# Performance work log

Measured on AMD Instinct MI355X. Metric: run time of the kernel, lower is better.

## Reference

```python
import jax, jax.numpy as jnp
import numpy as np

N = 100000      # n_heads + n_tails (graph nodes)
E = 1600000     # nnz of sparse adjacency A_in
D = 128         # in_dim == out_dim == embed_dim
LAMDA = 0.5
ALPHA = 0.1
LAYER = 1
LN_EPS = 1e-5
LEAKY_SLOPE = 0.01


def setup_inputs() -> dict:
    key = jax.random.key(0)
    ks = jax.random.split(key, 12)
    glorot = lambda k, shape: jax.random.uniform(
        k, shape, jnp.float32, -1.0, 1.0) * np.sqrt(6.0 / (shape[0] + shape[1]))
    stdv = 1.0 / np.sqrt(D)
    return {
        "ego_embeddings": jax.random.normal(ks[0], (N, D), jnp.float32),
        "h0": jax.random.normal(ks[1], (N, D), jnp.float32),  # all_layers[0]
        "vals": jax.random.uniform(ks[2], (E,), jnp.float32),
        "row": jax.random.randint(ks[3], (E,), 0, N, jnp.int32),
        "col": jax.random.randint(ks[4], (E,), 0, N, jnp.int32),
        # nn.Parameter weight (in_dim, in_dim), uniform(-stdv, stdv)
        "weight": jax.random.uniform(ks[5], (D, D), jnp.float32, -stdv, stdv),
        # linear_h0: embed_dim -> in_dim
        "w_h0": glorot(ks[6], (D, D)),
        "b_h0": jnp.zeros((D,), jnp.float32),
        # linear: in_dim -> out_dim
        "w_lin": glorot(ks[7], (D, D)),
        "b_lin": jnp.zeros((D,), jnp.float32),
        # LayerNorm(out_dim)
        "gamma": jnp.ones((D,), jnp.float32),
        "beta_ln": jnp.zeros((D,), jnp.float32),
    }


def _layernorm(x, g, b):
    mu = jnp.mean(x, axis=-1, keepdims=True)
    var = jnp.mean(jnp.square(x - mu), axis=-1, keepdims=True)
    return (x - mu) * jax.lax.rsqrt(var + LN_EPS) * g + b


def reference(ego_embeddings, h0, vals, weight, w_h0, b_h0, w_lin, b_lin,
              gamma, beta_ln, row, col):
    n = ego_embeddings.shape[0]
    # side_embeddings = A_in @ ego_embeddings  (sparse COO SpMM)
    msgs = vals[:, None] * ego_embeddings[col]          # [E, D] gather
    side = jax.ops.segment_sum(msgs, row, num_segments=n)
    # gcn aggregator
    hi = ego_embeddings + side
    # residual_connection with identity mapping (GCNII-style)
    h0p = h0 @ w_h0.T + b_h0
    residual = (1.0 - ALPHA) * hi + ALPHA * h0p
    beta = float(np.log(LAMDA / LAYER + 1.0))
    identity_mapping = (1.0 - beta) + beta * weight     # [D, D]
    emb = residual @ identity_mapping
    # linear + LeakyReLU
    emb = jax.nn.leaky_relu(emb @ w_lin.T + b_lin, LEAKY_SLOPE)
    # LayerNorm; dropout p=0 -> identity
    return _layernorm(emb, gamma, beta_ln)
```

## Files before the change

### kernel.cpp

```cpp
#include <hip/hip_runtime.h>

#define DD 128
#define SLOTS 64

typedef float  nf4 __attribute__((ext_vector_type(4)));
typedef int    ni4 __attribute__((ext_vector_type(4)));

__global__ void scatter_k(const int* __restrict__ rowi, const int* __restrict__ coli,
                          const float* __restrict__ vals, int* __restrict__ cnt,
                          int2* __restrict__ edgeS, int E) {
  int e = (blockIdx.x * 256 + threadIdx.x) * 4;
  if (e + 3 < E) {
    ni4 r = __builtin_nontemporal_load((const ni4*)(rowi + e));
    ni4 c = __builtin_nontemporal_load((const ni4*)(coli + e));
    nf4 v = __builtin_nontemporal_load((const nf4*)(vals + e));
    int p0 = atomicAdd(&cnt[r.x], 1);
    int p1 = atomicAdd(&cnt[r.y], 1);
    int p2 = atomicAdd(&cnt[r.z], 1);
    int p3 = atomicAdd(&cnt[r.w], 1);
    if (p0 < SLOTS) edgeS[(size_t)r.x * SLOTS + p0] = make_int2(c.x, __float_as_int(v.x));
    if (p1 < SLOTS) edgeS[(size_t)r.y * SLOTS + p1] = make_int2(c.y, __float_as_int(v.y));
    if (p2 < SLOTS) edgeS[(size_t)r.z * SLOTS + p2] = make_int2(c.z, __float_as_int(v.z));
    if (p3 < SLOTS) edgeS[(size_t)r.w * SLOTS + p3] = make_int2(c.w, __float_as_int(v.w));
  } else {
    for (int j = 0; j < 4; ++j) {
      if (e + j < E) {
        int r = rowi[e + j];
        int p = atomicAdd(&cnt[r], 1);
        if (p < SLOTS) edgeS[(size_t)r * SLOTS + p] =
            make_int2(coli[e + j], __float_as_int(vals[e + j]));
      }
    }
  }
}

__global__ void w2_k(const float* __restrict__ weight, const float* __restrict__ w_lin,
                     float* __restrict__ W2) {
  const float BETA = 0.40546510810816438f;
  int idx = blockIdx.x * 256 + threadIdx.x;
  int i = idx >> 7, j = idx & 127;
  const float* wi = weight + i * DD;
  const float* lj = w_lin + j * DD;
  float s = 0.f;
#pragma unroll 8
  for (int k = 0; k < DD; ++k) s = fmaf(fmaf(BETA, wi[k], 1.0f - BETA), lj[k], s);
  W2[idx] = s;
}

__global__ void wt_k(const float* __restrict__ W2, const float* __restrict__ w_h0,
                     const float* __restrict__ b_h0, const float* __restrict__ b_lin,
                     float* __restrict__ Wf, float* __restrict__ cvec) {
  int idx = blockIdx.x * 256 + threadIdx.x;
  if (idx < 16384) {
    Wf[idx] = 0.9f * W2[idx];
  } else if (idx < 32768) {
    int t = idx - 16384;
    int p = t >> 7, n = t & 127;
    float s = 0.f;
#pragma unroll 8
    for (int k = 0; k < DD; ++k) s = fmaf(w_h0[k * DD + p], W2[k * DD + n], s);
    Wf[(128 + p) * DD + n] = 0.1f * s;
  } else if (idx < 32896) {
    int n = idx - 32768;
    float s = 0.f;
    for (int k = 0; k < DD; ++k) s = fmaf(b_h0[k], W2[k * DD + n], s);
    cvec[n] = fmaf(0.1f, s, b_lin[n]);
  }
}

__global__ __launch_bounds__(256) void fused_k(
    const float* __restrict__ ego, const int2* __restrict__ edgeS,
    const int* __restrict__ cntp, const float* __restrict__ h0,
    const float* __restrict__ Wf, const float* __restrict__ cvec,
    const float* __restrict__ gamma, const float* __restrict__ betaln,
    float* __restrict__ out, int n) {
  __shared__ float lds[4][1024];
  int wave = threadIdx.x >> 6;
  int lane = threadIdx.x & 63;
  int half = lane >> 5;
  int q = lane & 31;
  float* xs = &lds[wave][0];
  int row0 = blockIdx.x * 16 + wave * 4;
  const float4* eg4 = (const float4*)ego;
  const nf4* h4 = (const nf4*)h0;

#pragma unroll
  for (int t = 0; t < 4; ++t) {
    int r = row0 + t;
    if (r >= n) r = n - 1;
    float4 acc = (half == 0) ? eg4[(size_t)r * 32 + q] : (float4){0.f, 0.f, 0.f, 0.f};
    float4 acc2 = {0.f, 0.f, 0.f, 0.f};
    nf4 hrow = __builtin_nontemporal_load(h4 + (size_t)r * 32 + q);
    int cnt = cntp[r];
    if (cnt > SLOTS) cnt = SLOTS;
    const int2* row_edges = edgeS + (size_t)r * SLOTS;
    int mcol = 0;
    float mval = 0.f;
    if (lane < cnt) {
      int2 m = row_edges[lane];
      mcol = m.x;
      mval = __int_as_float(m.y);
    }
    int npair = (cnt + 1) >> 1;
    int j = 0;
    for (; j + 4 <= npair; j += 4) {
      int i0 = 2 * j + half;
      int c0 = __shfl(mcol, i0, 64);
      int c1 = __shfl(mcol, i0 + 2, 64);
      int c2 = __shfl(mcol, i0 + 4, 64);
      int c3 = __shfl(mcol, i0 + 6, 64);
      float v0 = __shfl(mval, i0, 64);
      float v1 = __shfl(mval, i0 + 2, 64);
      float v2 = __shfl(mval, i0 + 4, 64);
      float v3 = __shfl(mval, i0 + 6, 64);
      float4 g0 = eg4[(size_t)c0 * 32 + q];
      float4 g1 = eg4[(size_t)c1 * 32 + q];
      float4 g2 = eg4[(size_t)c2 * 32 + q];
      float4 g3 = eg4[(size_t)c3 * 32 + q];
      acc.x  = fmaf(v0, g0.x, acc.x);  acc.y  = fmaf(v0, g0.y, acc.y);
      acc.z  = fmaf(v0, g0.z, acc.z);  acc.w  = fmaf(v0, g0.w, acc.w);
      acc2.x = fmaf(v1, g1.x, acc2.x); acc2.y = fmaf(v1, g1.y, acc2.y);
      acc2.z = fmaf(v1, g1.z, acc2.z); acc2.w = fmaf(v1, g1.w, acc2.w);
      acc.x  = fmaf(v2, g2.x, acc.x);  acc.y  = fmaf(v2, g2.y, acc.y);
      acc.z  = fmaf(v2, g2.z, acc.z);  acc.w  = fmaf(v2, g2.w, acc.w);
      acc2.x = fmaf(v3, g3.x, acc2.x); acc2.y = fmaf(v3, g3.y, acc2.y);
      acc2.z = fmaf(v3, g3.z, acc2.z); acc2.w = fmaf(v3, g3.w, acc2.w);
    }
    if (j + 2 <= npair) {
      int i0 = 2 * j + half;
      int c0 = __shfl(mcol, i0, 64);
      int c1 = __shfl(mcol, i0 + 2, 64);
      float v0 = __shfl(mval, i0, 64);
      float v1 = __shfl(mval, i0 + 2, 64);
      float4 g0 = eg4[(size_t)c0 * 32 + q];
      float4 g1 = eg4[(size_t)c1 * 32 + q];
      acc.x  = fmaf(v0, g0.x, acc.x);  acc.y  = fmaf(v0, g0.y, acc.y);
      acc.z  = fmaf(v0, g0.z, acc.z);  acc.w  = fmaf(v0, g0.w, acc.w);
      acc2.x = fmaf(v1, g1.x, acc2.x); acc2.y = fmaf(v1, g1.y, acc2.y);
      acc2.z = fmaf(v1, g1.z, acc2.z); acc2.w = fmaf(v1, g1.w, acc2.w);
      j += 2;
    }
    if (j < npair) {
      int i0 = 2 * j + half;
      int c0 = __shfl(mcol, i0, 64);
      float v0 = __shfl(mval, i0, 64);
      float4 g0 = eg4[(size_t)c0 * 32 + q];
      acc.x = fmaf(v0, g0.x, acc.x); acc.y = fmaf(v0, g0.y, acc.y);
      acc.z = fmaf(v0, g0.z, acc.z); acc.w = fmaf(v0, g0.w, acc.w);
    }
    acc.x += acc2.x; acc.y += acc2.y; acc.z += acc2.z; acc.w += acc2.w;
    acc.x += __shfl_xor(acc.x, 32, 64);
    acc.y += __shfl_xor(acc.y, 32, 64);
    acc.z += __shfl_xor(acc.z, 32, 64);
    acc.w += __shfl_xor(acc.w, 32, 64);
    if (half == 0) {
      *(float4*)(xs + t * 256 + 4 * q) = acc;
    } else {
      *(float4*)(xs + t * 256 + 128 + 4 * q) =
          (float4){hrow.x, hrow.y, hrow.z, hrow.w};
    }
  }

  float acc0[4], acc1[4];
#pragma unroll
  for (int r = 0; r < 4; ++r) { acc0[r] = 0.f; acc1[r] = 0.f; }

  for (int kb = 0; kb < 64; ++kb) {
    int k = kb * 4;
    float wA0 = Wf[(k + 0) * DD + lane];
    float wA1 = Wf[(k + 1) * DD + lane];
    float wA2 = Wf[(k + 2) * DD + lane];
    float wA3 = Wf[(k + 3) * DD + lane];
    float wB0 = Wf[(k + 0) * DD + 64 + lane];
    float wB1 = Wf[(k + 1) * DD + 64 + lane];
    float wB2 = Wf[(k + 2) * DD + 64 + lane];
    float wB3 = Wf[(k + 3) * DD + 64 + lane];
#pragma unroll
    for (int r = 0; r < 4; ++r) {
      float4 xv = *(const float4*)(xs + r * 256 + k);
      acc0[r] = fmaf(xv.x, wA0, acc0[r]);
      acc0[r] = fmaf(xv.y, wA1, acc0[r]);
      acc0[r] = fmaf(xv.z, wA2, acc0[r]);
      acc0[r] = fmaf(xv.w, wA3, acc0[r]);
      acc1[r] = fmaf(xv.x, wB0, acc1[r]);
      acc1[r] = fmaf(xv.y, wB1, acc1[r]);
      acc1[r] = fmaf(xv.z, wB2, acc1[r]);
      acc1[r] = fmaf(xv.w, wB3, acc1[r]);
    }
  }

  float cb0 = cvec[lane], cb1 = cvec[64 + lane];
#pragma unroll
  for (int r = 0; r < 4; ++r) {
    float t0 = acc0[r] + cb0;
    t0 = (t0 > 0.f) ? t0 : 0.01f * t0;
    float t1 = acc1[r] + cb1;
    t1 = (t1 > 0.f) ? t1 : 0.01f * t1;
    xs[r * 132 + lane] = t0;
    xs[r * 132 + 64 + lane] = t1;
  }

  int r = lane >> 4, p = lane & 15;
  const float* base = xs + r * 132 + p * 8;
  float4 va[2];
  float s = 0.f, qq = 0.f;
#pragma unroll
  for (int j = 0; j < 2; ++j) {
    float4 t = *(const float4*)(base + j * 4);
    va[j] = t;
    s += t.x + t.y + t.z + t.w;
    qq = fmaf(t.x, t.x, qq);
    qq = fmaf(t.y, t.y, qq);
    qq = fmaf(t.z, t.z, qq);
    qq = fmaf(t.w, t.w, qq);
  }
  s += __shfl_xor(s, 1, 64);
  s += __shfl_xor(s, 2, 64);
  s += __shfl_xor(s, 4, 64);
  s += __shfl_xor(s, 8, 64);
  qq += __shfl_xor(qq, 1, 64);
  qq += __shfl_xor(qq, 2, 64);
  qq += __shfl_xor(qq, 4, 64);
  qq += __shfl_xor(qq, 8, 64);
  float mean = s * (1.f / 128.f);
  float var = fmaf(qq, 1.f / 128.f, -mean * mean);
  float rstd = rsqrtf(var + 1e-5f);

  int orow = row0 + r;
  if (orow < n) {
    float* op = out + (size_t)orow * DD + p * 8;
    const float* gp = gamma + p * 8;
    const float* bp = betaln + p * 8;
#pragma unroll
    for (int j = 0; j < 2; ++j) {
      float4 g = *(const float4*)(gp + j * 4);
      float4 b = *(const float4*)(bp + j * 4);
      nf4 o;
      o.x = fmaf((va[j].x - mean) * rstd, g.x, b.x);
      o.y = fmaf((va[j].y - mean) * rstd, g.y, b.y);
      o.z = fmaf((va[j].z - mean) * rstd, g.z, b.z);
      o.w = fmaf((va[j].w - mean) * rstd, g.w, b.w);
      __builtin_nontemporal_store(o, (nf4*)(op + j * 4));
    }
  }
}

extern "C" void kernel_launch(void* const* d_in, const int* in_sizes, int n_in,
                              void* d_out, int out_size, void* d_ws, size_t ws_size,
                              hipStream_t stream) {
  const float* ego    = (const float*)d_in[0];
  const float* h0     = (const float*)d_in[1];
  const float* vals   = (const float*)d_in[2];
  const int*   rowi   = (const int*)d_in[3];
  const int*   coli   = (const int*)d_in[4];
  const float* weight = (const float*)d_in[5];
  const float* w_h0   = (const float*)d_in[6];
  const float* b_h0   = (const float*)d_in[7];
  const float* w_lin  = (const float*)d_in[8];
  const float* b_lin  = (const float*)d_in[9];
  const float* gamma  = (const float*)d_in[10];
  const float* betaln = (const float*)d_in[11];

  const int N = in_sizes[0] / DD;
  const int E = in_sizes[2];

  char* p = (char*)d_ws;
  auto carve = [&](size_t bytes) {
    char* q = p;
    p += (bytes + 255) & ~(size_t)255;
    return q;
  };
  int*   cnt   = (int*)carve((size_t)N * 4);
  float* W2    = (float*)carve(16384 * 4);
  float* Wf    = (float*)carve(32768 * 4);
  float* cvec  = (float*)carve(128 * 4);
  int2*  edgeS = (int2*)carve((size_t)N * SLOTS * 8);
  (void)n_in; (void)out_size; (void)ws_size;

  float* outf = (float*)d_out;

  (void)hipMemsetAsync(cnt, 0, (size_t)N * 4, stream);
  scatter_k<<<(E + 1023) / 1024, 256, 0, stream>>>(rowi, coli, vals, cnt, edgeS, E);
  w2_k<<<64, 256, 0, stream>>>(weight, w_lin, W2);
  wt_k<<<129, 256, 0, stream>>>(W2, w_h0, b_h0, b_lin, Wf, cvec);
  fused_k<<<(N + 15) / 16, 256, 0, stream>>>(ego, edgeS, cnt, h0, Wf, cvec,
                                             gamma, betaln, outf, N);
}
```

Before: 355.9 us.

## Fuse all stages into one persistent cooperative kernel with grid syncs

```diff
diff --git a/kernel.cpp b/kernel.cpp
--- a/kernel.cpp
+++ b/kernel.cpp
@@ -1,10 +1,240 @@
 #include <hip/hip_runtime.h>
+#include <hip/hip_cooperative_groups.h>
+
+namespace cg = cooperative_groups;
 
 #define DD 128
 #define SLOTS 64
 
 typedef float  nf4 __attribute__((ext_vector_type(4)));
 typedef int    ni4 __attribute__((ext_vector_type(4)));
+
+__global__ __launch_bounds__(256) void mega_k(
+    const float* __restrict__ ego, const int* __restrict__ rowi,
+    const int* __restrict__ coli, const float* __restrict__ vals,
+    const float* __restrict__ h0, const float* __restrict__ weight,
+    const float* __restrict__ w_h0, const float* __restrict__ b_h0,
+    const float* __restrict__ w_lin, const float* __restrict__ b_lin,
+    const float* __restrict__ gamma, const float* __restrict__ betaln,
+    int* __restrict__ cnt, int2* __restrict__ edgeS, float* __restrict__ W2,
+    float* __restrict__ Wf, float* __restrict__ cvec, float* __restrict__ out,
+    int n, int E) {
+  __shared__ float lds[4][1024];
+  cg::grid_group gg = cg::this_grid();
+  const int gsz = (int)(gridDim.x * 256);
+  const int gtid = (int)(blockIdx.x * 256 + threadIdx.x);
+
+  for (int i = gtid; i < n; i += gsz) cnt[i] = 0;
+  gg.sync();
+
+  for (int e = gtid; e < E; e += gsz) {
+    int r = rowi[e];
+    int p = atomicAdd(&cnt[r], 1);
+    if (p < SLOTS) edgeS[(size_t)r * SLOTS + p] = make_int2(coli[e], __float_as_int(vals[e]));
+  }
+  {
+    const float BETA = 0.40546510810816438f;
+    for (int idx = gtid; idx < 16384; idx += gsz) {
+      int i = idx >> 7, j = idx & 127;
+      const float* wi = weight + i * DD;
+      const float* lj = w_lin + j * DD;
+      float s = 0.f;
+#pragma unroll 8
+      for (int k = 0; k < DD; ++k) s = fmaf(fmaf(BETA, wi[k], 1.0f - BETA), lj[k], s);
+      W2[idx] = s;
+    }
+  }
+  gg.sync();
+
+  for (int idx = gtid; idx < 32896; idx += gsz) {
+    if (idx < 16384) {
+      Wf[idx] = 0.9f * W2[idx];
+    } else if (idx < 32768) {
+      int t = idx - 16384;
+      int p = t >> 7, nn = t & 127;
+      float s = 0.f;
+#pragma unroll 8
+      for (int k = 0; k < DD; ++k) s = fmaf(w_h0[k * DD + p], W2[k * DD + nn], s);
+      Wf[(128 + p) * DD + nn] = 0.1f * s;
+    } else {
+      int nn = idx - 32768;
+      float s = 0.f;
+      for (int k = 0; k < DD; ++k) s = fmaf(b_h0[k], W2[k * DD + nn], s);
+      cvec[nn] = fmaf(0.1f, s, b_lin[nn]);
+    }
+  }
+  gg.sync();
+
+  int wave = threadIdx.x >> 6;
+  int lane = threadIdx.x & 63;
+  int half = lane >> 5;
+  int q = lane & 31;
+  float* xs = &lds[wave][0];
+  const float4* eg4 = (const float4*)ego;
+  const nf4* h4 = (const nf4*)h0;
+  int ntiles = (n + 15) / 16;
+
+  for (int tile = blockIdx.x; tile < ntiles; tile += gridDim.x) {
+    int row0 = tile * 16 + wave * 4;
+
+#pragma unroll
+    for (int t = 0; t < 4; ++t) {
+      int r = row0 + t;
+      if (r >= n) r = n - 1;
+      float4 acc = (half == 0) ? eg4[(size_t)r * 32 + q] : (float4){0.f, 0.f, 0.f, 0.f};
+      float4 acc2 = {0.f, 0.f, 0.f, 0.f};
+      nf4 hrow = __builtin_nontemporal_load(h4 + (size_t)r * 32 + q);
+      int c = cnt[r];
+      if (c > SLOTS) c = SLOTS;
+      const int2* row_edges = edgeS + (size_t)r * SLOTS;
+      int mcol = 0;
+      float mval = 0.f;
+      if (lane < c) {
+        int2 m = row_edges[lane];
+        mcol = m.x;
+        mval = __int_as_float(m.y);
+      }
+      int npair = (c + 1) >> 1;
+      int j = 0;
+      for (; j + 4 <= npair; j += 4) {
+        int i0 = 2 * j + half;
+        int c0 = __shfl(mcol, i0, 64);
+        int c1 = __shfl(mcol, i0 + 2, 64);
+        int c2 = __shfl(mcol, i0 + 4, 64);
+        int c3 = __shfl(mcol, i0 + 6, 64);
+        float v0 = __shfl(mval, i0, 64);
+        float v1 = __shfl(mval, i0 + 2, 64);
+        float v2 = __shfl(mval, i0 + 4, 64);
+        float v3 = __shfl(mval, i0 + 6, 64);
+        float4 g0 = eg4[(size_t)c0 * 32 + q];
+        float4 g1 = eg4[(size_t)c1 * 32 + q];
+        float4 g2 = eg4[(size_t)c2 * 32 + q];
+        float4 g3 = eg4[(size_t)c3 * 32 + q];
+        acc.x  = fmaf(v0, g0.x, acc.x);  acc.y  = fmaf(v0, g0.y, acc.y);
+        acc.z  = fmaf(v0, g0.z, acc.z);  acc.w  = fmaf(v0, g0.w, acc.w);
+        acc2.x = fmaf(v1, g1.x, acc2.x); acc2.y = fmaf(v1, g1.y, acc2.y);
+        acc2.z = fmaf(v1, g1.z, acc2.z); acc2.w = fmaf(v1, g1.w, acc2.w);
+        acc.x  = fmaf(v2, g2.x, acc.x);  acc.y  = fmaf(v2, g2.y, acc.y);
+        acc.z  = fmaf(v2, g2.z, acc.z);  acc.w  = fmaf(v2, g2.w, acc.w);
+        acc2.x = fmaf(v3, g3.x, acc2.x); acc2.y = fmaf(v3, g3.y, acc2.y);
+        acc2.z = fmaf(v3, g3.z, acc2.z); acc2.w = fmaf(v3, g3.w, acc2.w);
+      }
+      if (j + 2 <= npair) {
+        int i0 = 2 * j + half;
+        int c0 = __shfl(mcol, i0, 64);
+        int c1 = __shfl(mcol, i0 + 2, 64);
+        float v0 = __shfl(mval, i0, 64);
+        float v1 = __shfl(mval, i0 + 2, 64);
+        float4 g0 = eg4[(size_t)c0 * 32 + q];
+        float4 g1 = eg4[(size_t)c1 * 32 + q];
+        acc.x  = fmaf(v0, g0.x, acc.x);  acc.y  = fmaf(v0, g0.y, acc.y);
+        acc.z  = fmaf(v0, g0.z, acc.z);  acc.w  = fmaf(v0, g0.w, acc.w);
+        acc2.x = fmaf(v1, g1.x, acc2.x); acc2.y = fmaf(v1, g1.y, acc2.y);
+        acc2.z = fmaf(v1, g1.z, acc2.z); acc2.w = fmaf(v1, g1.w, acc2.w);
+        j += 2;
+      }
+      if (j < npair) {
+        int i0 = 2 * j + half;
+        int c0 = __shfl(mcol, i0, 64);
+        float v0 = __shfl(mval, i0, 64);
+        float4 g0 = eg4[(size_t)c0 * 32 + q];
+        acc.x = fmaf(v0, g0.x, acc.x); acc.y = fmaf(v0, g0.y, acc.y);
+        acc.z = fmaf(v0, g0.z, acc.z); acc.w = fmaf(v0, g0.w, acc.w);
+      }
+      acc.x += acc2.x; acc.y += acc2.y; acc.z += acc2.z; acc.w += acc2.w;
+      acc.x += __shfl_xor(acc.x, 32, 64);
+      acc.y += __shfl_xor(acc.y, 32, 64);
+      acc.z += __shfl_xor(acc.z, 32, 64);
+      acc.w += __shfl_xor(acc.w, 32, 64);
+      if (half == 0) {
+        *(float4*)(xs + t * 256 + 4 * q) = acc;
+      } else {
+        *(float4*)(xs + t * 256 + 128 + 4 * q) = (float4){hrow.x, hrow.y, hrow.z, hrow.w};
+      }
+    }
+
+    float acc0[4], acc1[4];
+#pragma unroll
+    for (int r = 0; r < 4; ++r) { acc0[r] = 0.f; acc1[r] = 0.f; }
+    for (int kb = 0; kb < 64; ++kb) {
+      int k = kb * 4;
+      float wA0 = Wf[(k + 0) * DD + lane];
+      float wA1 = Wf[(k + 1) * DD + lane];
+      float wA2 = Wf[(k + 2) * DD + lane];
+      float wA3 = Wf[(k + 3) * DD + lane];
+      float wB0 = Wf[(k + 0) * DD + 64 + lane];
+      float wB1 = Wf[(k + 1) * DD + 64 + lane];
+      float wB2 = Wf[(k + 2) * DD + 64 + lane];
+      float wB3 = Wf[(k + 3) * DD + 64 + lane];
+#pragma unroll
+      for (int r = 0; r < 4; ++r) {
+        float4 xv = *(const float4*)(xs + r * 256 + k);
+        acc0[r] = fmaf(xv.x, wA0, acc0[r]);
+        acc0[r] = fmaf(xv.y, wA1, acc0[r]);
+        acc0[r] = fmaf(xv.z, wA2, acc0[r]);
+        acc0[r] = fmaf(xv.w, wA3, acc0[r]);
+        acc1[r] = fmaf(xv.x, wB0, acc1[r]);
+        acc1[r] = fmaf(xv.y, wB1, acc1[r]);
+        acc1[r] = fmaf(xv.z, wB2, acc1[r]);
+        acc1[r] = fmaf(xv.w, wB3, acc1[r]);
+      }
+    }
+
+    float cb0 = cvec[lane], cb1 = cvec[64 + lane];
+#pragma unroll
+    for (int r = 0; r < 4; ++r) {
+      float t0 = acc0[r] + cb0;
+      t0 = (t0 > 0.f) ? t0 : 0.01f * t0;
+      float t1 = acc1[r] + cb1;
+      t1 = (t1 > 0.f) ? t1 : 0.01f * t1;
+      xs[r * 132 + lane] = t0;
+      xs[r * 132 + 64 + lane] = t1;
+    }
+
+    int r = lane >> 4, p = lane & 15;
+    const float* base = xs + r * 132 + p * 8;
+    float4 va[2];
+    float s = 0.f, qq = 0.f;
+#pragma unroll
+    for (int j2 = 0; j2 < 2; ++j2) {
+      float4 t = *(const float4*)(base + j2 * 4);
+      va[j2] = t;
+      s += t.x + t.y + t.z + t.w;
+      qq = fmaf(t.x, t.x, qq);
+      qq = fmaf(t.y, t.y, qq);
+      qq = fmaf(t.z, t.z, qq);
+      qq = fmaf(t.w, t.w, qq);
+    }
+    s += __shfl_xor(s, 1, 64);
+    s += __shfl_xor(s, 2, 64);
+    s += __shfl_xor(s, 4, 64);
+    s += __shfl_xor(s, 8, 64);
+    qq += __shfl_xor(qq, 1, 64);
+    qq += __shfl_xor(qq, 2, 64);
+    qq += __shfl_xor(qq, 4, 64);
+    qq += __shfl_xor(qq, 8, 64);
+    float mean = s * (1.f / 128.f);
+    float var = fmaf(qq, 1.f / 128.f, -mean * mean);
+    float rstd = rsqrtf(var + 1e-5f);
+    int orow = tile * 16 + wave * 4 + r;
+    if (orow < n) {
+      float* op = out + (size_t)orow * DD + p * 8;
+      const float* gp = gamma + p * 8;
+      const float* bp = betaln + p * 8;
+#pragma unroll
+      for (int j2 = 0; j2 < 2; ++j2) {
+        float4 g = *(const float4*)(gp + j2 * 4);
+        float4 b = *(const float4*)(bp + j2 * 4);
+        nf4 o;
+        o.x = fmaf((va[j2].x - mean) * rstd, g.x, b.x);
+        o.y = fmaf((va[j2].y - mean) * rstd, g.y, b.y);
+        o.z = fmaf((va[j2].z - mean) * rstd, g.z, b.z);
+        o.w = fmaf((va[j2].w - mean) * rstd, g.w, b.w);
+        __builtin_nontemporal_store(o, (nf4*)(op + j2 * 4));
+      }
+    }
+  }
+}
 
 __global__ void scatter_k(const int* __restrict__ rowi, const int* __restrict__ coli,
                           const float* __restrict__ vals, int* __restrict__ cnt,
@@ -83,7 +313,6 @@
   int row0 = blockIdx.x * 16 + wave * 4;
   const float4* eg4 = (const float4*)ego;
   const nf4* h4 = (const nf4*)h0;
-
 #pragma unroll
   for (int t = 0; t < 4; ++t) {
     int r = row0 + t;
@@ -156,15 +385,12 @@
     if (half == 0) {
       *(float4*)(xs + t * 256 + 4 * q) = acc;
     } else {
-      *(float4*)(xs + t * 256 + 128 + 4 * q) =
-          (float4){hrow.x, hrow.y, hrow.z, hrow.w};
-    }
-  }
-
+      *(float4*)(xs + t * 256 + 128 + 4 * q) = (float4){hrow.x, hrow.y, hrow.z, hrow.w};
+    }
+  }
   float acc0[4], acc1[4];
 #pragma unroll
   for (int r = 0; r < 4; ++r) { acc0[r] = 0.f; acc1[r] = 0.f; }
-
   for (int kb = 0; kb < 64; ++kb) {
     int k = kb * 4;
     float wA0 = Wf[(k + 0) * DD + lane];
@@ -188,7 +414,6 @@
       acc1[r] = fmaf(xv.w, wB3, acc1[r]);
     }
   }
-
   float cb0 = cvec[lane], cb1 = cvec[64 + lane];
 #pragma unroll
   for (int r = 0; r < 4; ++r) {
@@ -199,7 +424,6 @@
     xs[r * 132 + lane] = t0;
     xs[r * 132 + 64 + lane] = t1;
   }
-
   int r = lane >> 4, p = lane & 15;
   const float* base = xs + r * 132 + p * 8;
   float4 va[2];
@@ -225,7 +449,6 @@
   float mean = s * (1.f / 128.f);
   float var = fmaf(qq, 1.f / 128.f, -mean * mean);
   float rstd = rsqrtf(var + 1e-5f);
-
   int orow = row0 + r;
   if (orow < n) {
     float* op = out + (size_t)orow * DD + p * 8;
@@ -261,8 +484,8 @@
   const float* gamma  = (const float*)d_in[10];
   const float* betaln = (const float*)d_in[11];
 
-  const int N = in_sizes[0] / DD;
-  const int E = in_sizes[2];
+  int N = in_sizes[0] / DD;
+  int E = in_sizes[2];
 
   char* p = (char*)d_ws;
   auto carve = [&](size_t bytes) {
@@ -279,6 +502,28 @@
 
   float* outf = (float*)d_out;
 
+  int dev = 0;
+  (void)hipGetDevice(&dev);
+  hipDeviceProp_t prop;
+  hipError_t perr = hipGetDeviceProperties(&prop, dev);
+  int maxB = 0;
+  hipError_t oerr = hipOccupancyMaxActiveBlocksPerMultiprocessor(&maxB, mega_k, 256, 0);
+  bool coop_ok = (perr == hipSuccess) && (oerr == hipSuccess) && (maxB > 0) &&
+                 (prop.cooperativeLaunch != 0);
+  if (coop_ok) {
+    int grid = maxB * prop.multiProcessorCount;
+    int ntiles = (N + 15) / 16;
+    if (grid > ntiles) grid = ntiles;
+    void* kargs[] = {(void*)&ego,   (void*)&rowi,  (void*)&coli,  (void*)&vals,
+                     (void*)&h0,    (void*)&weight,(void*)&w_h0,  (void*)&b_h0,
+                     (void*)&w_lin, (void*)&b_lin, (void*)&gamma, (void*)&betaln,
+                     (void*)&cnt,   (void*)&edgeS, (void*)&W2,    (void*)&Wf,
+                     (void*)&cvec,  (void*)&outf,  (void*)&N,     (void*)&E};
+    hipError_t lerr = hipLaunchCooperativeKernel((const void*)mega_k, dim3(grid),
+                                                 dim3(256), kargs, 0, stream);
+    if (lerr == hipSuccess) return;
+  }
+
   (void)hipMemsetAsync(cnt, 0, (size_t)N * 4, stream);
   scatter_k<<<(E + 1023) / 1024, 256, 0, stream>>>(rowi, coli, vals, cnt, edgeS, E);
   w2_k<<<64, 256, 0, stream>>>(weight, w_lin, W2);
```

New measurement: 553.3 us. 1.55x slower.
